# Kernel optimization log

Hardware: AMD Instinct MI355X
Metric: run time of the kernel (lower is better)

Reference implementation:

```python
import jax, jax.numpy as jnp
import numpy as np

B, C, U, LEN, K = 32, 16, 16, 128, 4  # batch, channels, units, image side, cheb order
POWERS = K + 1


def _path_chebyshev(n, k):
    """Chebyshev polynomials T_0..T_k of the rescaled normalized Laplacian of an
    undirected path graph with n nodes. Returns [k+1, n, n] float32."""
    A = np.zeros((n, n), dtype=np.float64)
    A[np.arange(n - 1), np.arange(1, n)] = 1.0
    A = A + A.T
    d = A.sum(axis=1)
    dinv = 1.0 / np.sqrt(d)
    L = np.eye(n) - dinv[:, None] * A * dinv[None, :]   # normalized Laplacian
    Lt = L - np.eye(n)                                   # rescaled: 2L/lambda_max - I, lambda_max=2
    T = [np.eye(n), Lt]
    for _ in range(2, k + 1):
        T.append(2.0 * Lt @ T[-1] - T[-2])
    return np.stack(T[: k + 1]).astype(np.float32)


def setup_inputs() -> dict:
    key = jax.random.key(0)
    kx, kc = jax.random.split(key)
    x = jax.random.normal(kx, (B, C, LEN, LEN), dtype=jnp.float32)
    coefs = 0.001 * jax.random.normal(kc, (POWERS, POWERS, C, U), dtype=jnp.float32)
    cheb = jnp.asarray(_path_chebyshev(LEN, K))  # same graph for both axes
    return {"x": x, "coefs": coefs, "cheb1": cheb, "cheb2": cheb}


def reference(x, coefs, cheb1, cheb2):
    # out[b,u,p,q] = sum_{k1,k2,c,h,w} coefs[k1,k2,c,u] * cheb1[k1,h,p] * x[b,c,h,w] * cheb2[k2,w,q]
    t1 = jnp.einsum('bchw,khp->bkcpw', x, cheb1)        # apply cheb1 along H
    s = jnp.einsum('bkcpw,klcu->blupw', t1, coefs)      # contract k1 and channels
    out = jnp.einsum('blupw,lwq->bupq', s, cheb2)       # apply cheb2 along W, contract k2
    return out
```

## Files before the change

### kernel.cpp

```cpp
#include <hip/hip_runtime.h>
#include <hip/hip_bf16.h>

#define LEN 128
#define NB 32
#define NC 16
#define NU 16
#define NK 5
#define KC 80
#define KCP 96
#define LUN 80

typedef unsigned int uint32;
typedef unsigned short ushort16;
typedef __attribute__((ext_vector_type(8))) short bf16x8;
typedef __attribute__((ext_vector_type(4))) float f32x4;

#define MFMA(a, b, c) __builtin_amdgcn_mfma_f32_16x16x32_bf16(a, b, c, 0, 0, 0)

#define SIG(r) (((r) & 15) ^ (((r) >> 3) & 15))

static __device__ inline ushort16 f2bf(float f) {
    union { float f; uint32 u; } v; v.f = f;
    uint32 u = v.u;
    uint32 r = (u + 0x7fffu + ((u >> 16) & 1u)) >> 16;
    return (ushort16)r;
}
static __device__ inline uint32 pkbf(float a, float b) {
    return (uint32)f2bf(a) | ((uint32)f2bf(b) << 16);
}
static __device__ inline bf16x8 frag16(const void* p) {
    return *(const bf16x8*)p;
}

__global__ __launch_bounds__(256) void k0_prep(const float* __restrict__ coefs,
                                               const float* __restrict__ cheb1,
                                               const float* __restrict__ cheb2,
                                               ushort16* __restrict__ cheb1T,
                                               ushort16* __restrict__ cheb2T,
                                               ushort16* __restrict__ coefTT) {
    int i = blockIdx.x * 256 + threadIdx.x;
    if (i < 81920) {
        int kp = i >> 7, h = i & 127;
        int k = kp >> 7, p = kp & 127;
        cheb1T[i] = f2bf(cheb1[(k * LEN + h) * LEN + p]);
    } else if (i < 163840) {
        int j = i - 81920;
        int q = j / 640, t = j % 640;
        int l = t >> 7, w = t & 127;
        cheb2T[j] = f2bf(cheb2[(l * LEN + w) * LEN + q]);
    } else if (i < 171520) {
        int j = i - 163840;
        int lu = j / KCP, kc = j % KCP;
        int l = lu >> 4, u = lu & 15, k = kc >> 4, c = kc & 15;
        coefTT[j] = (kc < KC) ? f2bf(coefs[((k * NK + l) * NC + c) * NU + u]) : (ushort16)0;
    }
}

__global__ __launch_bounds__(256, 2) void k1_mfma(const float* __restrict__ x,
                                                  const uint32* __restrict__ cheb1T,
                                                  ushort16* __restrict__ t1, int b0) {
    __shared__ __align__(16) uint32 Xs[128 * 64];
    __shared__ __align__(16) uint32 As[160 * 64];
    const int c = blockIdx.x, bl = blockIdx.y, b = b0 + bl;
    const int tid = threadIdx.x;
    const int lane = tid & 63, wave = tid >> 6;
    const int m16 = lane & 15, g = lane >> 4;
    const int wm = wave >> 1, wn = wave & 1;

    {
        const float* xp = x + (size_t)(b * NC + c) * (LEN * LEN);
        int w = tid & 127, hg = tid >> 7;
        #pragma unroll
        for (int uu = 0; uu < 8; ++uu) {
            int u = hg * 8 + uu;
            uint4 d;
            uint32* dp = (uint32*)&d;
            #pragma unroll
            for (int t = 0; t < 4; ++t) {
                int h2 = u * 4 + t;
                dp[t] = pkbf(xp[(2 * h2) * LEN + w], xp[(2 * h2 + 1) * LEN + w]);
            }
            *(uint4*)(Xs + w * 64 + ((u ^ SIG(w)) << 2)) = d;
        }
    }

    for (int pass = 0; pass < 4; ++pass) {
        __syncthreads();
        #pragma unroll
        for (int i = 0; i < 10; ++i) {
            int it = tid + i * 256;
            int r = it >> 4, cc = it & 15;
            uint4 v = *(const uint4*)(cheb1T + (size_t)(pass * 160 + r) * 64 + cc * 4);
            *(uint4*)(As + r * 64 + ((cc ^ SIG(r)) << 2)) = v;
        }
        __syncthreads();

        f32x4 acc[4][5];
        #pragma unroll
        for (int mi = 0; mi < 4; ++mi)
            #pragma unroll
            for (int ni = 0; ni < 5; ++ni) acc[mi][ni] = (f32x4)0.f;

        #pragma unroll
        for (int ks = 0; ks < 4; ++ks) {
            bf16x8 Af[4], Bf[5];
            #pragma unroll
            for (int mi = 0; mi < 4; ++mi) {
                int row = wm * 64 + mi * 16 + m16;
                Af[mi] = frag16(Xs + row * 64 + (((ks * 4 + g) ^ SIG(row)) << 2));
            }
            #pragma unroll
            for (int ni = 0; ni < 5; ++ni) {
                int row = wn * 80 + ni * 16 + m16;
                Bf[ni] = frag16(As + row * 64 + (((ks * 4 + g) ^ SIG(row)) << 2));
            }
            #pragma unroll
            for (int mi = 0; mi < 4; ++mi)
                #pragma unroll
                for (int ni = 0; ni < 5; ++ni)
                    acc[mi][ni] = MFMA(Af[mi], Bf[ni], acc[mi][ni]);
        }

        #pragma unroll
        for (int ni = 0; ni < 5; ++ni) {
            int kp = pass * 160 + wn * 80 + ni * 16 + m16;
            int k = kp >> 7, p = kp & 127;
            size_t base = (((size_t)(bl * LEN + p) * NK + k) * NC + c) * LEN;
            #pragma unroll
            for (int mi = 0; mi < 4; ++mi) {
                int w0 = wm * 64 + mi * 16 + g * 4;
                uint2 d;
                d.x = pkbf(acc[mi][ni][0], acc[mi][ni][1]);
                d.y = pkbf(acc[mi][ni][2], acc[mi][ni][3]);
                *(uint2*)((ushort16*)t1 + base + w0) = d;
            }
        }
    }
}

__global__ __launch_bounds__(256, 2) void k2_mfma(const ushort16* __restrict__ t1,
                                                  const ushort16* __restrict__ coefTT,
                                                  const ushort16* __restrict__ cheb2T,
                                                  float* __restrict__ out, int b0) {
    __shared__ __align__(16) uint32 sm[2 * 128 * 64];
    const int pg = blockIdx.x, bl = blockIdx.y, b = b0 + bl;
    const int tid = threadIdx.x;
    const int lane = tid & 63, wave = tid >> 6;
    const int n16 = lane & 15, g = lane >> 4;

    {
        const uint32* t1u = (const uint32*)(t1 + (size_t)(bl * LEN + 2 * pg) * (KC * LEN));
        #pragma unroll
        for (int i = 0; i < 5; ++i) {
            int it = tid + i * 256;
            int p_i = (it >= 640) ? 1 : 0;
            int rem = it - 640 * p_i;
            int kc2 = rem >> 4, wq = rem & 15;
            const uint32* src = t1u + p_i * 5120 + kc2 * 128 + wq * 4;
            uint4 Av = *(const uint4*)(src);
            uint4 Bv = *(const uint4*)(src + 64);
            const uint32* av = (const uint32*)&Av;
            const uint32* bv = (const uint32*)&Bv;
            int u = kc2 >> 2, lo = kc2 & 3;
            #pragma unroll
            for (int j = 0; j < 4; ++j) {
                int r0 = p_i * 128 + wq * 8 + 2 * j;
                int r1 = r0 + 1;
                sm[r0 * 64 + ((u ^ SIG(r0)) << 2) + lo] = (av[j] & 0xffffu) | (bv[j] << 16);
                sm[r1 * 64 + ((u ^ SIG(r1)) << 2) + lo] = (av[j] >> 16) | (bv[j] & 0xffff0000u);
            }
        }
        for (int j = tid; j < 2048; j += 256) {
            int row = j >> 3, d = j & 7;
            int u = 10 + (d >> 2);
            sm[row * 64 + ((u ^ SIG(row)) << 2) + (d & 3)] = 0;
        }
    }
    __syncthreads();

    const int wp = wave >> 1, ww = wave & 1;
    f32x4 acc[4][5];
    #pragma unroll
    for (int mi = 0; mi < 4; ++mi)
        #pragma unroll
        for (int ni = 0; ni < 5; ++ni) acc[mi][ni] = (f32x4)0.f;

    #pragma unroll
    for (int ks = 0; ks < 3; ++ks) {
        bf16x8 Af[4], Bf[5];
        #pragma unroll
        for (int mi = 0; mi < 4; ++mi) {
            int row = wp * 128 + ww * 64 + mi * 16 + n16;
            Af[mi] = frag16(sm + row * 64 + (((ks * 4 + g) ^ SIG(row)) << 2));
        }
        #pragma unroll
        for (int ni = 0; ni < 5; ++ni)
            Bf[ni] = frag16(coefTT + (size_t)(ni * 16 + n16) * KCP + ks * 32 + g * 8);
        #pragma unroll
        for (int mi = 0; mi < 4; ++mi)
            #pragma unroll
            for (int ni = 0; ni < 5; ++ni)
                acc[mi][ni] = MFMA(Af[mi], Bf[ni], acc[mi][ni]);
    }
    __syncthreads();

    {
        ushort16* A3 = (ushort16*)sm;
        #pragma unroll
        for (int mi = 0; mi < 4; ++mi)
            #pragma unroll
            for (int ni = 0; ni < 5; ++ni) {
                int lu = ni * 16 + n16, u = lu & 15, l = lu >> 4;
                int w0 = ww * 64 + mi * 16 + g * 4;
                int pu = wp * 16 + u;
                uint2 d;
                d.x = pkbf(acc[mi][ni][0], acc[mi][ni][1]);
                d.y = pkbf(acc[mi][ni][2], acc[mi][ni][3]);
                *(uint2*)(A3 + pu * 648 + l * 128 + w0) = d;
            }
    }
    __syncthreads();

    const ushort16* A3r = (const ushort16*)sm;
    f32x4 c3[2][2];
    c3[0][0] = (f32x4)0.f; c3[0][1] = (f32x4)0.f;
    c3[1][0] = (f32x4)0.f; c3[1][1] = (f32x4)0.f;
    #pragma unroll 5
    for (int ks = 0; ks < 20; ++ks) {
        bf16x8 Af2[2], Bf2[2];
        #pragma unroll
        for (int mi = 0; mi < 2; ++mi)
            Af2[mi] = frag16(A3r + (mi * 16 + n16) * 648 + ks * 32 + g * 8);
        #pragma unroll
        for (int nt = 0; nt < 2; ++nt)
            Bf2[nt] = frag16(cheb2T + (size_t)(wave * 32 + nt * 16 + n16) * 640 + ks * 32 + g * 8);
        #pragma unroll
        for (int mi = 0; mi < 2; ++mi)
            #pragma unroll
            for (int nt = 0; nt < 2; ++nt)
                c3[mi][nt] = MFMA(Af2[mi], Bf2[nt], c3[mi][nt]);
    }

    #pragma unroll
    for (int mi = 0; mi < 2; ++mi)
        #pragma unroll
        for (int nt = 0; nt < 2; ++nt)
            #pragma unroll
            for (int r = 0; r < 4; ++r) {
                int u = g * 4 + r;
                int q = wave * 32 + nt * 16 + n16;
                out[(((size_t)(b * NU + u)) * LEN + (2 * pg + mi)) * LEN + q] = c3[mi][nt][r];
            }
}

extern "C" void kernel_launch(void* const* d_in, const int* in_sizes, int n_in,
                              void* d_out, int out_size, void* d_ws, size_t ws_size,
                              hipStream_t stream) {
    const float* x     = (const float*)d_in[0];
    const float* coefs = (const float*)d_in[1];
    const float* cheb1 = (const float*)d_in[2];
    const float* cheb2 = (const float*)d_in[3];
    float* out = (float*)d_out;

    const size_t aux_bytes = 163840 + 163840 + 15360;
    size_t aux_off = (ws_size - aux_bytes) & ~(size_t)255;
    ushort16* cheb1T = (ushort16*)((char*)d_ws + aux_off);
    ushort16* cheb2T = cheb1T + 81920;
    ushort16* coefTT = cheb2T + 81920;
    ushort16* t1 = (ushort16*)d_ws;

    const size_t per_b = (size_t)NK * NC * LEN * LEN * sizeof(ushort16);
    int chunk = (int)(aux_off / per_b);
    if (chunk < 1) chunk = 1;
    if (chunk > NB) chunk = NB;

    hipLaunchKernelGGL(k0_prep, dim3((171520 + 255) / 256), dim3(256), 0, stream,
                       coefs, cheb1, cheb2, cheb1T, cheb2T, coefTT);
    for (int b0 = 0; b0 < NB; b0 += chunk) {
        int cb = (NB - b0 < chunk) ? (NB - b0) : chunk;
        hipLaunchKernelGGL(k1_mfma, dim3(NC, cb), dim3(256), 0, stream,
                           x, (const uint32*)cheb1T, t1, b0);
        hipLaunchKernelGGL(k2_mfma, dim3(64, cb), dim3(256), 0, stream,
                           t1, coefTT, cheb2T, out, b0);
    }
}
```

Before: 172.7 us.

## Prepack operands in MFMA fragment order and split stage-one work across more blocks

Adds a separate prep kernel that converts x to bf16 and stores it in MFMA fragment order. The Chebyshev and coefficient tables are also prepacked into per-lane fragment order, so the matmul kernels can load fragments straight from global memory instead of staging them in shared memory. Stage one now splits the output columns across a third grid dimension, giving eight times as many smaller blocks. It stages results in LDS so t1 is written with coalesced 16-byte stores. Stage two processes one row per block with less shared memory and higher occupancy, at the cost of an extra kernel launch and an extra round trip of x through memory.

```diff
diff --git a/kernel.cpp b/kernel.cpp
--- a/kernel.cpp
+++ b/kernel.cpp
@@ -8,7 +8,6 @@
 #define NK 5
 #define KC 80
 #define KCP 96
-#define LUN 80
 
 typedef unsigned int uint32;
 typedef unsigned short ushort16;
@@ -35,40 +34,43 @@
 __global__ __launch_bounds__(256) void k0_prep(const float* __restrict__ coefs,
                                                const float* __restrict__ cheb1,
                                                const float* __restrict__ cheb2,
-                                               ushort16* __restrict__ cheb1T,
-                                               ushort16* __restrict__ cheb2T,
-                                               ushort16* __restrict__ coefTT) {
+                                               ushort16* __restrict__ cheb1F,
+                                               ushort16* __restrict__ cheb2F,
+                                               ushort16* __restrict__ coefF) {
     int i = blockIdx.x * 256 + threadIdx.x;
     if (i < 81920) {
-        int kp = i >> 7, h = i & 127;
+        int j = i & 7, lane = (i >> 3) & 63, ks = (i >> 9) & 3, nt = i >> 11;
+        int kp = nt * 16 + (lane & 15);
         int k = kp >> 7, p = kp & 127;
-        cheb1T[i] = f2bf(cheb1[(k * LEN + h) * LEN + p]);
+        int h = ks * 32 + ((lane >> 4) << 3) + j;
+        cheb1F[i] = f2bf(cheb1[(k * LEN + h) * LEN + p]);
     } else if (i < 163840) {
-        int j = i - 81920;
-        int q = j / 640, t = j % 640;
-        int l = t >> 7, w = t & 127;
-        cheb2T[j] = f2bf(cheb2[(l * LEN + w) * LEN + q]);
+        int i2 = i - 81920;
+        int j = i2 & 7, lane = (i2 >> 3) & 63, t = i2 >> 9;
+        int ks = t % 20, nt = t / 20;
+        int q = nt * 16 + (lane & 15);
+        int lw = ks * 32 + ((lane >> 4) << 3) + j;
+        int l = lw >> 7, w = lw & 127;
+        cheb2F[i2] = f2bf(cheb2[(l * LEN + w) * LEN + q]);
     } else if (i < 171520) {
-        int j = i - 163840;
-        int lu = j / KCP, kc = j % KCP;
-        int l = lu >> 4, u = lu & 15, k = kc >> 4, c = kc & 15;
-        coefTT[j] = (kc < KC) ? f2bf(coefs[((k * NK + l) * NC + c) * NU + u]) : (ushort16)0;
-    }
-}
-
-__global__ __launch_bounds__(256, 2) void k1_mfma(const float* __restrict__ x,
-                                                  const uint32* __restrict__ cheb1T,
-                                                  ushort16* __restrict__ t1, int b0) {
+        int i3 = i - 163840;
+        int j = i3 & 7, lane = (i3 >> 3) & 63, t = i3 >> 9;
+        int ks = t % 3, nt = t / 3;
+        int lu = nt * 16 + (lane & 15);
+        int l = lu >> 4, u = lu & 15;
+        int kc = ks * 32 + ((lane >> 4) << 3) + j;
+        int k = kc >> 4, c = kc & 15;
+        coefF[i3] = (kc < KC) ? f2bf(coefs[((k * NK + l) * NC + c) * NU + u]) : (ushort16)0;
+    }
+}
+
+__global__ __launch_bounds__(256) void kx_prep(const float* __restrict__ x,
+                                               ushort16* __restrict__ xF) {
     __shared__ __align__(16) uint32 Xs[128 * 64];
-    __shared__ __align__(16) uint32 As[160 * 64];
-    const int c = blockIdx.x, bl = blockIdx.y, b = b0 + bl;
+    const int bc = blockIdx.x;
     const int tid = threadIdx.x;
-    const int lane = tid & 63, wave = tid >> 6;
-    const int m16 = lane & 15, g = lane >> 4;
-    const int wm = wave >> 1, wn = wave & 1;
-
+    const float* xp = x + (size_t)bc * (LEN * LEN);
     {
-        const float* xp = x + (size_t)(b * NC + c) * (LEN * LEN);
         int w = tid & 127, hg = tid >> 7;
         #pragma unroll
         for (int uu = 0; uu < 8; ++uu) {
@@ -83,174 +85,185 @@
             *(uint4*)(Xs + w * 64 + ((u ^ SIG(w)) << 2)) = d;
         }
     }
-
-    for (int pass = 0; pass < 4; ++pass) {
-        __syncthreads();
-        #pragma unroll
-        for (int i = 0; i < 10; ++i) {
+    __syncthreads();
+    ushort16* dst = xF + (size_t)bc * 16384;
+    #pragma unroll
+    for (int i = 0; i < 8; ++i) {
+        int n = tid + i * 256;
+        int lane = n & 63, fk = n >> 6;
+        int wrow = (fk >> 2) * 16 + (lane & 15);
+        int u = (fk & 3) * 4 + (lane >> 4);
+        uint4 v = *(const uint4*)(Xs + wrow * 64 + ((u ^ SIG(wrow)) << 2));
+        *(uint4*)(dst + (size_t)n * 8) = v;
+    }
+}
+
+__global__ __launch_bounds__(256, 4) void k1_mfma(const ushort16* __restrict__ xF,
+                                                  const ushort16* __restrict__ cheb1F,
+                                                  ushort16* __restrict__ t1, int b0) {
+    __shared__ __align__(16) uint32 Bs[80 * 64];
+    const int c = blockIdx.x, bl = blockIdx.y, ns = blockIdx.z;
+    const int b = b0 + bl;
+    const int tid = threadIdx.x;
+    const int lane = tid & 63, wm = tid >> 6;
+    const int m16 = lane & 15, g = lane >> 4;
+
+    const ushort16* xFb = xF + ((size_t)(b * NC + c)) * 16384;
+
+    f32x4 acc[2][5];
+    #pragma unroll
+    for (int mi = 0; mi < 2; ++mi)
+        #pragma unroll
+        for (int ni = 0; ni < 5; ++ni) acc[mi][ni] = (f32x4)0.f;
+
+    #pragma unroll
+    for (int ks = 0; ks < 4; ++ks) {
+        bf16x8 Af[2], Bf[5];
+        #pragma unroll
+        for (int mi = 0; mi < 2; ++mi) {
+            int mt = wm * 2 + mi;
+            Af[mi] = frag16(xFb + ((size_t)(mt * 4 + ks) * 64 + lane) * 8);
+        }
+        #pragma unroll
+        for (int ni = 0; ni < 5; ++ni) {
+            int nt = ns * 5 + ni;
+            Bf[ni] = frag16(cheb1F + ((size_t)(nt * 4 + ks) * 64 + lane) * 8);
+        }
+        #pragma unroll
+        for (int mi = 0; mi < 2; ++mi)
+            #pragma unroll
+            for (int ni = 0; ni < 5; ++ni)
+                acc[mi][ni] = MFMA(Af[mi], Bf[ni], acc[mi][ni]);
+    }
+
+    #pragma unroll
+    for (int ni = 0; ni < 5; ++ni)
+        #pragma unroll
+        for (int mi = 0; mi < 2; ++mi) {
+            int rr = ni * 16 + m16;
+            int wu = wm * 32 + mi * 16 + g * 4;
+            uint2 d;
+            d.x = pkbf(acc[mi][ni][0], acc[mi][ni][1]);
+            d.y = pkbf(acc[mi][ni][2], acc[mi][ni][3]);
+            int u = wu >> 3;
+            *(uint2*)(Bs + rr * 64 + ((u ^ SIG(rr)) << 2) + ((wu >> 1) & 3)) = d;
+        }
+    __syncthreads();
+
+    #pragma unroll
+    for (int i = 0; i < 5; ++i) {
+        int n = tid + i * 256;
+        int rr = n >> 4, wsg = n & 15;
+        uint4 v = *(const uint4*)(Bs + rr * 64 + ((wsg ^ SIG(rr)) << 2));
+        int kp = ns * 80 + rr;
+        int k = kp >> 7, p = kp & 127;
+        *(uint4*)(t1 + ((size_t)((bl * LEN + p) * KC + k * NC + c)) * LEN + wsg * 8) = v;
+    }
+}
+
+__global__ __launch_bounds__(256, 4) void k2_mfma(const ushort16* __restrict__ t1,
+                                                  const ushort16* __restrict__ coefF,
+                                                  const ushort16* __restrict__ cheb2F,
+                                                  float* __restrict__ out, int b0) {
+    __shared__ __align__(16) uint32 sm[128 * 64];
+    const int p = blockIdx.x, bl = blockIdx.y, b = b0 + bl;
+    const int tid = threadIdx.x;
+    const int lane = tid & 63, wave = tid >> 6;
+    const int n16 = lane & 15, g = lane >> 4;
+
+    {
+        const uint32* t1u = (const uint32*)(t1 + (size_t)(bl * LEN + p) * (KC * LEN));
+        #pragma unroll
+        for (int i = 0; i < 3; ++i) {
             int it = tid + i * 256;
-            int r = it >> 4, cc = it & 15;
-            uint4 v = *(const uint4*)(cheb1T + (size_t)(pass * 160 + r) * 64 + cc * 4);
-            *(uint4*)(As + r * 64 + ((cc ^ SIG(r)) << 2)) = v;
-        }
-        __syncthreads();
-
-        f32x4 acc[4][5];
-        #pragma unroll
-        for (int mi = 0; mi < 4; ++mi)
+            if (it < 640) {
+                int a = it >> 4, wq = it & 15;
+                const uint32* src = t1u + (2 * a) * 64 + wq * 4;
+                uint4 Av = *(const uint4*)(src);
+                uint4 Bv = *(const uint4*)(src + 64);
+                const uint32* av = (const uint32*)&Av;
+                const uint32* bv = (const uint32*)&Bv;
+                int u = a >> 2, lo = a & 3;
+                #pragma unroll
+                for (int j = 0; j < 4; ++j) {
+                    int r0 = wq * 8 + 2 * j, r1 = r0 + 1;
+                    sm[r0 * 64 + ((u ^ SIG(r0)) << 2) + lo] = (av[j] & 0xffffu) | (bv[j] << 16);
+                    sm[r1 * 64 + ((u ^ SIG(r1)) << 2) + lo] = (av[j] >> 16) | (bv[j] & 0xffff0000u);
+                }
+            }
+        }
+        #pragma unroll
+        for (int i = 0; i < 4; ++i) {
+            int idx = tid + i * 256;
+            int row = idx >> 3, d = idx & 7;
+            int u = 10 + (d >> 2);
+            sm[row * 64 + ((u ^ SIG(row)) << 2) + (d & 3)] = 0;
+        }
+    }
+    __syncthreads();
+
+    f32x4 acc[2][5];
+    #pragma unroll
+    for (int mi = 0; mi < 2; ++mi)
+        #pragma unroll
+        for (int ni = 0; ni < 5; ++ni) acc[mi][ni] = (f32x4)0.f;
+
+    #pragma unroll
+    for (int ks = 0; ks < 3; ++ks) {
+        bf16x8 Af[2], Bf[5];
+        #pragma unroll
+        for (int mi = 0; mi < 2; ++mi) {
+            int row = wave * 32 + mi * 16 + n16;
+            int uu = ks * 4 + g;
+            Af[mi] = frag16(sm + row * 64 + ((uu ^ SIG(row)) << 2));
+        }
+        #pragma unroll
+        for (int ni = 0; ni < 5; ++ni)
+            Bf[ni] = frag16(coefF + ((size_t)(ni * 3 + ks) * 64 + lane) * 8);
+        #pragma unroll
+        for (int mi = 0; mi < 2; ++mi)
             #pragma unroll
-            for (int ni = 0; ni < 5; ++ni) acc[mi][ni] = (f32x4)0.f;
-
-        #pragma unroll
-        for (int ks = 0; ks < 4; ++ks) {
-            bf16x8 Af[4], Bf[5];
-            #pragma unroll
-            for (int mi = 0; mi < 4; ++mi) {
-                int row = wm * 64 + mi * 16 + m16;
-                Af[mi] = frag16(Xs + row * 64 + (((ks * 4 + g) ^ SIG(row)) << 2));
-            }
+            for (int ni = 0; ni < 5; ++ni)
+                acc[mi][ni] = MFMA(Af[mi], Bf[ni], acc[mi][ni]);
+    }
+    __syncthreads();
+
+    {
+        ushort16* A3 = (ushort16*)sm;
+        #pragma unroll
+        for (int mi = 0; mi < 2; ++mi)
             #pragma unroll
             for (int ni = 0; ni < 5; ++ni) {
-                int row = wn * 80 + ni * 16 + m16;
-                Bf[ni] = frag16(As + row * 64 + (((ks * 4 + g) ^ SIG(row)) << 2));
-            }
-            #pragma unroll
-            for (int mi = 0; mi < 4; ++mi)
-                #pragma unroll
-                for (int ni = 0; ni < 5; ++ni)
-                    acc[mi][ni] = MFMA(Af[mi], Bf[ni], acc[mi][ni]);
-        }
-
-        #pragma unroll
-        for (int ni = 0; ni < 5; ++ni) {
-            int kp = pass * 160 + wn * 80 + ni * 16 + m16;
-            int k = kp >> 7, p = kp & 127;
-            size_t base = (((size_t)(bl * LEN + p) * NK + k) * NC + c) * LEN;
-            #pragma unroll
-            for (int mi = 0; mi < 4; ++mi) {
-                int w0 = wm * 64 + mi * 16 + g * 4;
+                int wcol = wave * 32 + mi * 16 + g * 4;
                 uint2 d;
                 d.x = pkbf(acc[mi][ni][0], acc[mi][ni][1]);
                 d.y = pkbf(acc[mi][ni][2], acc[mi][ni][3]);
-                *(uint2*)((ushort16*)t1 + base + w0) = d;
+                *(uint2*)(A3 + n16 * 648 + ni * 128 + wcol) = d;
             }
-        }
-    }
-}
-
-__global__ __launch_bounds__(256, 2) void k2_mfma(const ushort16* __restrict__ t1,
-                                                  const ushort16* __restrict__ coefTT,
-                                                  const ushort16* __restrict__ cheb2T,
-                                                  float* __restrict__ out, int b0) {
-    __shared__ __align__(16) uint32 sm[2 * 128 * 64];
-    const int pg = blockIdx.x, bl = blockIdx.y, b = b0 + bl;
-    const int tid = threadIdx.x;
-    const int lane = tid & 63, wave = tid >> 6;
-    const int n16 = lane & 15, g = lane >> 4;
-
-    {
-        const uint32* t1u = (const uint32*)(t1 + (size_t)(bl * LEN + 2 * pg) * (KC * LEN));
-        #pragma unroll
-        for (int i = 0; i < 5; ++i) {
-            int it = tid + i * 256;
-            int p_i = (it >= 640) ? 1 : 0;
-            int rem = it - 640 * p_i;
-            int kc2 = rem >> 4, wq = rem & 15;
-            const uint32* src = t1u + p_i * 5120 + kc2 * 128 + wq * 4;
-            uint4 Av = *(const uint4*)(src);
-            uint4 Bv = *(const uint4*)(src + 64);
-            const uint32* av = (const uint32*)&Av;
-            const uint32* bv = (const uint32*)&Bv;
-            int u = kc2 >> 2, lo = kc2 & 3;
-            #pragma unroll
-            for (int j = 0; j < 4; ++j) {
-                int r0 = p_i * 128 + wq * 8 + 2 * j;
-                int r1 = r0 + 1;
-                sm[r0 * 64 + ((u ^ SIG(r0)) << 2) + lo] = (av[j] & 0xffffu) | (bv[j] << 16);
-                sm[r1 * 64 + ((u ^ SIG(r1)) << 2) + lo] = (av[j] >> 16) | (bv[j] & 0xffff0000u);
-            }
-        }
-        for (int j = tid; j < 2048; j += 256) {
-            int row = j >> 3, d = j & 7;
-            int u = 10 + (d >> 2);
-            sm[row * 64 + ((u ^ SIG(row)) << 2) + (d & 3)] = 0;
-        }
-    }
-    __syncthreads();
-
-    const int wp = wave >> 1, ww = wave & 1;
-    f32x4 acc[4][5];
-    #pragma unroll
-    for (int mi = 0; mi < 4; ++mi)
-        #pragma unroll
-        for (int ni = 0; ni < 5; ++ni) acc[mi][ni] = (f32x4)0.f;
-
-    #pragma unroll
-    for (int ks = 0; ks < 3; ++ks) {
-        bf16x8 Af[4], Bf[5];
-        #pragma unroll
-        for (int mi = 0; mi < 4; ++mi) {
-            int row = wp * 128 + ww * 64 + mi * 16 + n16;
-            Af[mi] = frag16(sm + row * 64 + (((ks * 4 + g) ^ SIG(row)) << 2));
-        }
-        #pragma unroll
-        for (int ni = 0; ni < 5; ++ni)
-            Bf[ni] = frag16(coefTT + (size_t)(ni * 16 + n16) * KCP + ks * 32 + g * 8);
-        #pragma unroll
-        for (int mi = 0; mi < 4; ++mi)
-            #pragma unroll
-            for (int ni = 0; ni < 5; ++ni)
-                acc[mi][ni] = MFMA(Af[mi], Bf[ni], acc[mi][ni]);
-    }
-    __syncthreads();
-
-    {
-        ushort16* A3 = (ushort16*)sm;
-        #pragma unroll
-        for (int mi = 0; mi < 4; ++mi)
-            #pragma unroll
-            for (int ni = 0; ni < 5; ++ni) {
-                int lu = ni * 16 + n16, u = lu & 15, l = lu >> 4;
-                int w0 = ww * 64 + mi * 16 + g * 4;
-                int pu = wp * 16 + u;
-                uint2 d;
-                d.x = pkbf(acc[mi][ni][0], acc[mi][ni][1]);
-                d.y = pkbf(acc[mi][ni][2], acc[mi][ni][3]);
-                *(uint2*)(A3 + pu * 648 + l * 128 + w0) = d;
-            }
     }
     __syncthreads();
 
     const ushort16* A3r = (const ushort16*)sm;
-    f32x4 c3[2][2];
-    c3[0][0] = (f32x4)0.f; c3[0][1] = (f32x4)0.f;
-    c3[1][0] = (f32x4)0.f; c3[1][1] = (f32x4)0.f;
+    f32x4 c3[2];
+    c3[0] = (f32x4)0.f; c3[1] = (f32x4)0.f;
     #pragma unroll 5
     for (int ks = 0; ks < 20; ++ks) {
-        bf16x8 Af2[2], Bf2[2];
-        #pragma unroll
-        for (int mi = 0; mi < 2; ++mi)
-            Af2[mi] = frag16(A3r + (mi * 16 + n16) * 648 + ks * 32 + g * 8);
-        #pragma unroll
-        for (int nt = 0; nt < 2; ++nt)
-            Bf2[nt] = frag16(cheb2T + (size_t)(wave * 32 + nt * 16 + n16) * 640 + ks * 32 + g * 8);
-        #pragma unroll
-        for (int mi = 0; mi < 2; ++mi)
-            #pragma unroll
-            for (int nt = 0; nt < 2; ++nt)
-                c3[mi][nt] = MFMA(Af2[mi], Bf2[nt], c3[mi][nt]);
-    }
-
-    #pragma unroll
-    for (int mi = 0; mi < 2; ++mi)
-        #pragma unroll
-        for (int nt = 0; nt < 2; ++nt)
-            #pragma unroll
-            for (int r = 0; r < 4; ++r) {
-                int u = g * 4 + r;
-                int q = wave * 32 + nt * 16 + n16;
-                out[(((size_t)(b * NU + u)) * LEN + (2 * pg + mi)) * LEN + q] = c3[mi][nt][r];
-            }
+        bf16x8 Aa = frag16(A3r + n16 * 648 + ks * 32 + g * 8);
+        #pragma unroll
+        for (int nt = 0; nt < 2; ++nt) {
+            bf16x8 Bb = frag16(cheb2F + ((size_t)((wave * 2 + nt) * 20 + ks) * 64 + lane) * 8);
+            c3[nt] = MFMA(Aa, Bb, c3[nt]);
+        }
+    }
+
+    #pragma unroll
+    for (int nt = 0; nt < 2; ++nt)
+        #pragma unroll
+        for (int r = 0; r < 4; ++r) {
+            int u = g * 4 + r;
+            int q = wave * 32 + nt * 16 + n16;
+            out[(((size_t)(b * NU + u)) * LEN + p) * LEN + q] = c3[nt][r];
+        }
 }
 
 extern "C" void kernel_launch(void* const* d_in, const int* in_sizes, int n_in,
@@ -262,25 +275,28 @@
     const float* cheb2 = (const float*)d_in[3];
     float* out = (float*)d_out;
 
+    const size_t xF_bytes  = (size_t)NB * NC * 16384 * sizeof(ushort16);
     const size_t aux_bytes = 163840 + 163840 + 15360;
-    size_t aux_off = (ws_size - aux_bytes) & ~(size_t)255;
-    ushort16* cheb1T = (ushort16*)((char*)d_ws + aux_off);
-    ushort16* cheb2T = cheb1T + 81920;
-    ushort16* coefTT = cheb2T + 81920;
+    size_t off = (ws_size - aux_bytes - xF_bytes) & ~(size_t)255;
+    ushort16* cheb1F = (ushort16*)((char*)d_ws + off);
+    ushort16* cheb2F = cheb1F + 81920;
+    ushort16* coefF  = cheb2F + 81920;
+    ushort16* xF     = coefF + 7680;
     ushort16* t1 = (ushort16*)d_ws;
 
-    const size_t per_b = (size_t)NK * NC * LEN * LEN * sizeof(ushort16);
-    int chunk = (int)(aux_off / per_b);
+    const size_t per_b = (size_t)LEN * KC * LEN * sizeof(ushort16);
+    int chunk = (int)(off / per_b);
     if (chunk < 1) chunk = 1;
     if (chunk > NB) chunk = NB;
 
-    hipLaunchKernelGGL(k0_prep, dim3((171520 + 255) / 256), dim3(256), 0, stream,
-                       coefs, cheb1, cheb2, cheb1T, cheb2T, coefTT);
+    hipLaunchKernelGGL(k0_prep, dim3(171520 / 256), dim3(256), 0, stream,
+                       coefs, cheb1, cheb2, cheb1F, cheb2F, coefF);
+    hipLaunchKernelGGL(kx_prep, dim3(NB * NC), dim3(256), 0, stream, x, xF);
     for (int b0 = 0; b0 < NB; b0 += chunk) {
         int cb = (NB - b0 < chunk) ? (NB - b0) : chunk;
-        hipLaunchKernelGGL(k1_mfma, dim3(NC, cb), dim3(256), 0, stream,
-                           x, (const uint32*)cheb1T, t1, b0);
-        hipLaunchKernelGGL(k2_mfma, dim3(64, cb), dim3(256), 0, stream,
-                           t1, coefTT, cheb2T, out, b0);
-    }
-}
+        hipLaunchKernelGGL(k1_mfma, dim3(NC, cb, 8), dim3(256), 0, stream,
+                           xF, cheb1F, t1, b0);
+        hipLaunchKernelGGL(k2_mfma, dim3(LEN, cb), dim3(256), 0, stream,
+                           t1, coefF, cheb2F, out, b0);
+    }
+}
```

Result: faster. 151.0 us (-12.6%).
